# Performance work log

Hardware: AMD Instinct MI355X
Metric: run time of the kernel (lower is better)

Reference implementation:

```python
import jax, jax.numpy as jnp
import numpy as np

ALPHA = 0.2  # LeakyReLU negative slope
NEG_INF = -9e15


def setup_inputs() -> dict:
    key = jax.random.key(0)
    k1, k2, k3, k4 = jax.random.split(key, 4)
    N, IN_F, OUT_F = 8192, 512, 256
    h = jax.random.normal(k1, (N, IN_F), dtype=jnp.float32)
    adj = jax.random.randint(k2, (N, N), 0, 2).astype(jnp.float32)
    # xavier_uniform for torch Linear weights
    limW = float(np.sqrt(6.0 / (IN_F + OUT_F)))
    W = jax.random.uniform(k3, (OUT_F, IN_F), dtype=jnp.float32, minval=-limW, maxval=limW)
    lima = float(np.sqrt(6.0 / (2 * OUT_F + 1)))
    a_vec = jax.random.uniform(k4, (2 * OUT_F,), dtype=jnp.float32, minval=-lima, maxval=lima)
    return {"h": h, "adj": adj, "W": W, "a_vec": a_vec}


def reference(h, adj, W, a_vec):
    # Wh = W(h), torch Linear: h @ W.T  -> [N, out]
    Wh = h @ W.T
    F_out = W.shape[0]
    # e_ij = leakyrelu(a . [Wh_i, Wh_j]) = leakyrelu(a1.Wh_i + a2.Wh_j)
    s_src = Wh @ a_vec[:F_out]   # [N] contribution of row i
    s_dst = Wh @ a_vec[F_out:]   # [N] contribution of col j
    e = jax.nn.leaky_relu(s_src[:, None] + s_dst[None, :], negative_slope=ALPHA)  # [N, N]
    scores = jnp.where(adj > 0, e, jnp.float32(NEG_INF))
    attention = jax.nn.softmax(scores, axis=1)
    # dropout is identity in eval mode
    h_prime = attention @ Wh  # [N, out]
    return h_prime, attention
```

## Files before the change

### kernel.cpp

```cpp
#include <hip/hip_runtime.h>
#include <stdint.h>

#define N_NODES 8192
#define IN_F    512
#define OUT_F   256
#define ALPHA   0.2f

typedef __attribute__((ext_vector_type(8))) short bf16x8;
typedef __attribute__((ext_vector_type(4))) float f32x4;

__device__ __forceinline__ uint32_t f32_to_bf16(float f) {
    union { float f; uint32_t u; } v; v.f = f;
    uint32_t u = v.u;
    return (u + 0x7fffu + ((u >> 16) & 1u)) >> 16;
}

__device__ __forceinline__ void async_copy16(const void* g, void* l) {
    __builtin_amdgcn_global_load_lds(
        (const __attribute__((address_space(1))) uint32_t*)g,
        (__attribute__((address_space(3))) uint32_t*)l, 16, 0, 0);
}

__global__ __launch_bounds__(256) void k0_wvec(
    const float* __restrict__ W, const float* __restrict__ a_vec,
    float* __restrict__ w12)
{
    const int t  = threadIdx.x;
    const int nb = blockIdx.x * 8;
    float a1lo = 0.f, a1hi = 0.f, a2lo = 0.f, a2hi = 0.f;
    #pragma unroll
    for (int q = 0; q < 8; q++) {
        int n = nb + q;
        float lo = W[(size_t)n * IN_F + t];
        float hi = W[(size_t)n * IN_F + t + 256];
        float a1 = a_vec[n], a2 = a_vec[OUT_F + n];
        a1lo = fmaf(lo, a1, a1lo); a1hi = fmaf(hi, a1, a1hi);
        a2lo = fmaf(lo, a2, a2lo); a2hi = fmaf(hi, a2, a2hi);
    }
    atomicAdd(&w12[t], a1lo);       atomicAdd(&w12[t + 256], a1hi);
    atomicAdd(&w12[512 + t], a2lo); atomicAdd(&w12[512 + t + 256], a2hi);
}

__global__ __launch_bounds__(256) void ks_svec(
    const float* __restrict__ h, const float* __restrict__ w12,
    float* __restrict__ s_src, float* __restrict__ s_dst)
{
    __shared__ float sw[1024];
    const int t = threadIdx.x;
    #pragma unroll
    for (int q = 0; q < 4; q++) sw[q * 256 + t] = w12[q * 256 + t];
    __syncthreads();
    const int w = t >> 6, ln = t & 63;
    const int i = blockIdx.x * 4 + w;
    const float* hr = h + (size_t)i * IN_F + ln * 8;
    float4 h0 = *(const float4*)hr;
    float4 h1 = *(const float4*)(hr + 4);
    const float* w1 = sw + ln * 8;
    const float* w2 = sw + 512 + ln * 8;
    float v1 = h0.x*w1[0] + h0.y*w1[1] + h0.z*w1[2] + h0.w*w1[3]
             + h1.x*w1[4] + h1.y*w1[5] + h1.z*w1[6] + h1.w*w1[7];
    float v2 = h0.x*w2[0] + h0.y*w2[1] + h0.z*w2[2] + h0.w*w2[3]
             + h1.x*w2[4] + h1.y*w2[5] + h1.z*w2[6] + h1.w*w2[7];
    #pragma unroll
    for (int off = 32; off >= 1; off >>= 1) {
        v1 += __shfl_xor(v1, off, 64);
        v2 += __shfl_xor(v2, off, 64);
    }
    if (ln == 0) { s_src[i] = v1; s_dst[i] = v2; }
}

__global__ __launch_bounds__(256) void k1_wh_pack(
    const float* __restrict__ h, const float* __restrict__ W,
    uint16_t* __restrict__ whf)
{
    const int n0 = blockIdx.x * 64, i0 = blockIdx.y * 64;
    const int t  = threadIdx.x;
    const int tn = t & 15, tm = t >> 4;

    __shared__ float As[32][65];
    __shared__ float Bs[32][65];

    float acc[4][4];
    #pragma unroll
    for (int i = 0; i < 4; i++)
        #pragma unroll
        for (int j = 0; j < 4; j++) acc[i][j] = 0.f;

    for (int k0 = 0; k0 < IN_F; k0 += 32) {
        __syncthreads();
        #pragma unroll
        for (int q = 0; q < 2; q++) {
            int u   = q * 256 + t;
            int row = u >> 3;
            int kf  = (u & 7) * 4;
            float4 va = *(const float4*)&h[(size_t)(i0 + row) * IN_F + k0 + kf];
            As[kf + 0][row] = va.x; As[kf + 1][row] = va.y;
            As[kf + 2][row] = va.z; As[kf + 3][row] = va.w;
            float4 vb = *(const float4*)&W[(size_t)(n0 + row) * IN_F + k0 + kf];
            Bs[kf + 0][row] = vb.x; Bs[kf + 1][row] = vb.y;
            Bs[kf + 2][row] = vb.z; Bs[kf + 3][row] = vb.w;
        }
        __syncthreads();
        #pragma unroll
        for (int kk = 0; kk < 32; kk++) {
            float a[4], b[4];
            *(float4*)a = *(const float4*)&As[kk][tm * 4];
            *(float4*)b = *(const float4*)&Bs[kk][tn * 4];
            #pragma unroll
            for (int i = 0; i < 4; i++)
                #pragma unroll
                for (int j = 0; j < 4; j++) acc[i][j] = fmaf(a[i], b[j], acc[i][j]);
        }
    }

    #pragma unroll
    for (int ii = 0; ii < 4; ii++) {
        int gr = i0 + tm * 4 + ii;
        int ck = gr >> 5;
        int lr = (gr >> 3) & 3;
        int jj = gr & 7;
        #pragma unroll
        for (int jn = 0; jn < 4; jn++) {
            int gc   = n0 + tn * 4 + jn;
            int c    = ck * 16 + (gc >> 4);
            int lane = (gc & 15) + lr * 16;
            whf[(size_t)c * 512 + lane * 8 + jj] = (uint16_t)f32_to_bf16(acc[ii][jn]);
        }
    }
}

__global__ __launch_bounds__(256) void k2_mask_l(
    const float* __restrict__ adj, const float* __restrict__ s_src,
    const float* __restrict__ s_dst, uint64_t* __restrict__ mask,
    float* __restrict__ l_out)
{
    const int i = blockIdx.x;
    const int t = threadIdx.x, w = t >> 6, ln = t & 63;
    const float si = s_src[i];
    const float4* rowv = (const float4*)(adj + (size_t)i * N_NODES);
    const float4* sdv  = (const float4*)s_dst;
    float acc = 0.f;
    #pragma unroll 2
    for (int it = 0; it < 8; it++) {
        int jb = it * 4 + w;
        int v4 = jb * 64 + ln;
        float4 a  = rowv[v4];
        float4 sd = sdv[v4];
        uint64_t b0 = __ballot(a.x > 0.f);
        uint64_t b1 = __ballot(a.y > 0.f);
        uint64_t b2 = __ballot(a.z > 0.f);
        uint64_t b3 = __ballot(a.w > 0.f);
        if (ln == 0) {
            uint64_t* mw = mask + (size_t)i * 128 + jb * 4;
            mw[0] = b0; mw[1] = b1; mw[2] = b2; mw[3] = b3;
        }
        float x, e;
        x = si + sd.x; e = fmaxf(x, ALPHA * x); if (a.x > 0.f) acc += __expf(e);
        x = si + sd.y; e = fmaxf(x, ALPHA * x); if (a.y > 0.f) acc += __expf(e);
        x = si + sd.z; e = fmaxf(x, ALPHA * x); if (a.z > 0.f) acc += __expf(e);
        x = si + sd.w; e = fmaxf(x, ALPHA * x); if (a.w > 0.f) acc += __expf(e);
    }
    #pragma unroll
    for (int off = 32; off >= 1; off >>= 1) acc += __shfl_xor(acc, off, 64);
    __shared__ float red[4];
    if (ln == 0) red[w] = acc;
    __syncthreads();
    if (t == 0) l_out[i] = (red[0] + red[1]) + (red[2] + red[3]);
}

__global__ __launch_bounds__(256) void k3_att_gemm(
    const uint64_t* __restrict__ mask, const float* __restrict__ s_src,
    const float* __restrict__ s_dst, const float* __restrict__ l_in,
    const uint16_t* __restrict__ whf, float* __restrict__ att_out,
    float* __restrict__ partial)
{
    const int rb = blockIdx.x, jc = blockIdx.y;
    const int i0 = rb * 32, jbase = jc * 2048;
    const int t = threadIdx.x, w = t >> 6, ln = t & 63;
    const int mh = w & 1, nh = w >> 1;

    __shared__ uint16_t whf_lds[16384];
    __shared__ uint64_t mw[2][32][4];
    __shared__ float    sd[2][64];
    __shared__ float    ssrc[32], invl[32];

    if (t < 32) { ssrc[t] = s_src[i0 + t]; invl[t] = 1.0f / l_in[i0 + t]; }
    if (t < 64) sd[0][t] = s_dst[jbase + t];
    if (t >= 64 && t < 192) {
        int r = (t - 64) >> 2, ph = t & 3;
        mw[0][r][ph] = mask[(size_t)(i0 + r) * 128 + (jbase >> 8) * 4 + ph];
    }

    f32x4 acc[8];
    #pragma unroll
    for (int b = 0; b < 8; b++) acc[b] = (f32x4){0.f, 0.f, 0.f, 0.f};

    const int m   = mh * 16 + (ln & 15);
    const int kof = (ln >> 4) * 8;

    int cur = 0;
    for (int it = 0; it < 32; it++) {
        const int j0 = jbase + it * 64;
        __syncthreads();

        const uint16_t* src = whf + (size_t)(j0 >> 5) * 8192;
        #pragma unroll
        for (int q = 0; q < 8; q++) {
            int c = w * 8 + q;
            async_copy16(src + (size_t)c * 512 + ln * 8, whf_lds + c * 512);
        }

        uint64_t mwv[4];
        #pragma unroll
        for (int ph = 0; ph < 4; ph++) mwv[ph] = mw[cur][m][ph];
        float sim = ssrc[m], il = invl[m];
        int bbase = ((it & 3) << 4) + (kof >> 2);
        float p[2][8];
        #pragma unroll
        for (int ks = 0; ks < 2; ks++) {
            #pragma unroll
            for (int jj = 0; jj < 8; jj++) {
                float x  = sim + sd[cur][ks * 32 + kof + jj];
                float e  = fmaxf(x, ALPHA * x);
                float pe = __expf(e) * il;
                int bidx = bbase + ks * 8 + (jj >> 2);
                p[ks][jj] = ((mwv[jj & 3] >> bidx) & 1ull) ? pe : 0.f;
            }
        }

        if (nh == 0) {
            float* go = att_out + (size_t)(i0 + m) * N_NODES + j0 + kof;
            __builtin_nontemporal_store(*(f32x4*)&p[0][0], (f32x4*)go);
            __builtin_nontemporal_store(*(f32x4*)&p[0][4], (f32x4*)(go + 4));
            __builtin_nontemporal_store(*(f32x4*)&p[1][0], (f32x4*)(go + 32));
            __builtin_nontemporal_store(*(f32x4*)&p[1][4], (f32x4*)(go + 36));
        }

        bf16x8 af[2];
        #pragma unroll
        for (int ks = 0; ks < 2; ks++) {
            union { bf16x8 v; uint32_t u[4]; } pk;
            #pragma unroll
            for (int q = 0; q < 4; q++)
                pk.u[q] = f32_to_bf16(p[ks][2 * q]) | (f32_to_bf16(p[ks][2 * q + 1]) << 16);
            af[ks] = pk.v;
        }

        if (it < 31) {
            int jn = j0 + 64;
            if (t < 64) sd[cur ^ 1][t] = s_dst[jn + t];
            else if (t < 192) {
                int r = (t - 64) >> 2, ph = t & 3;
                mw[cur ^ 1][r][ph] = mask[(size_t)(i0 + r) * 128 + (jn >> 8) * 4 + ph];
            }
        }
        __syncthreads();

        #pragma unroll
        for (int ks = 0; ks < 2; ks++) {
            #pragma unroll
            for (int nl = 0; nl < 8; nl++) {
                int nt = nh * 8 + nl;
                bf16x8 bfr = *(const bf16x8*)(whf_lds + (size_t)(ks * 16 + nt) * 512 + ln * 8);
                acc[nl] = __builtin_amdgcn_mfma_f32_16x16x32_bf16(af[ks], bfr, acc[nl], 0, 0, 0);
            }
        }
        cur ^= 1;
    }

    float* pbase = partial + (size_t)jc * ((size_t)N_NODES * OUT_F);
    int gr0 = i0 + mh * 16 + (ln >> 4) * 4;
    #pragma unroll
    for (int nl = 0; nl < 8; nl++) {
        int gc = nh * 128 + nl * 16 + (ln & 15);
        #pragma unroll
        for (int r = 0; r < 4; r++)
            pbase[(size_t)(gr0 + r) * OUT_F + gc] = acc[nl][r];
    }
}

__global__ __launch_bounds__(256) void k4_reduce(
    const float* __restrict__ partial, float* __restrict__ hp)
{
    const size_t S = (size_t)N_NODES * OUT_F;
    int idx = (blockIdx.x * 256 + threadIdx.x) * 4;
    float4 a = *(const float4*)(partial + idx);
    float4 b = *(const float4*)(partial + S + idx);
    float4 c = *(const float4*)(partial + 2 * S + idx);
    float4 d = *(const float4*)(partial + 3 * S + idx);
    float4 o;
    o.x = (a.x + b.x) + (c.x + d.x);
    o.y = (a.y + b.y) + (c.y + d.y);
    o.z = (a.z + b.z) + (c.z + d.z);
    o.w = (a.w + b.w) + (c.w + d.w);
    *(float4*)(hp + idx) = o;
}

extern "C" void kernel_launch(void* const* d_in, const int* in_sizes, int n_in,
                              void* d_out, int out_size, void* d_ws, size_t ws_size,
                              hipStream_t stream) {
    (void)in_sizes; (void)n_in; (void)out_size; (void)ws_size;
    const float* h     = (const float*)d_in[0];
    const float* adj   = (const float*)d_in[1];
    const float* W     = (const float*)d_in[2];
    const float* a_vec = (const float*)d_in[3];

    char* ws = (char*)d_ws;
    uint16_t* whf  = (uint16_t*)(ws);
    uint64_t* mask = (uint64_t*)(ws + ((size_t)4 << 20));
    float* partial = (float*)(ws + ((size_t)12 << 20));
    float* w12     = (float*)(ws + ((size_t)44 << 20));
    float* s_src   = (float*)(ws + ((size_t)44 << 20) + 16384);
    float* s_dst   = (float*)(ws + ((size_t)44 << 20) + 16384 + 32768);
    float* l_buf   = (float*)(ws + ((size_t)44 << 20) + 16384 + 65536);

    float* hp  = (float*)d_out;
    float* att = hp + (size_t)N_NODES * OUT_F;

    hipMemsetAsync(w12, 0, 4096, stream);
    k0_wvec<<<32, 256, 0, stream>>>(W, a_vec, w12);
    ks_svec<<<2048, 256, 0, stream>>>(h, w12, s_src, s_dst);
    k1_wh_pack<<<dim3(4, 128), 256, 0, stream>>>(h, W, whf);
    k2_mask_l<<<8192, 256, 0, stream>>>(adj, s_src, s_dst, mask, l_buf);
    k3_att_gemm<<<dim3(256, 4), 256, 0, stream>>>(mask, s_src, s_dst, l_buf, whf, att, partial);
    k4_reduce<<<2048, 256, 0, stream>>>(partial, hp);
}
```

Measured before the change: 645.0 us.

## Split K across waves in attention GEMM and drop LDS staging of Wh

The attention-GEMM kernel now splits each 64-column chunk across wave pairs along K instead of along N. Each wave computes its own 32 attention values and runs all 16 output column tiles, reading Wh fragments straight from global memory rather than through an async LDS copy. This removes the per-iteration block barriers and the redundant computation of softmax values, and adds a final LDS reduction between the two K halves. The trade-off is more global/L2 traffic for Wh, more accumulator registers (16 tiles, with an occupancy hint of 4), and padding of the k1 shared tiles to 68.

```diff
diff --git a/kernel.cpp b/kernel.cpp
--- a/kernel.cpp
+++ b/kernel.cpp
@@ -13,12 +13,6 @@
     union { float f; uint32_t u; } v; v.f = f;
     uint32_t u = v.u;
     return (u + 0x7fffu + ((u >> 16) & 1u)) >> 16;
-}
-
-__device__ __forceinline__ void async_copy16(const void* g, void* l) {
-    __builtin_amdgcn_global_load_lds(
-        (const __attribute__((address_space(1))) uint32_t*)g,
-        (__attribute__((address_space(3))) uint32_t*)l, 16, 0, 0);
 }
 
 __global__ __launch_bounds__(256) void k0_wvec(
@@ -77,8 +71,8 @@
     const int t  = threadIdx.x;
     const int tn = t & 15, tm = t >> 4;
 
-    __shared__ float As[32][65];
-    __shared__ float Bs[32][65];
+    __shared__ float As[32][68];
+    __shared__ float Bs[32][68];
 
     float acc[4][4];
     #pragma unroll
@@ -168,7 +162,7 @@
     if (t == 0) l_out[i] = (red[0] + red[1]) + (red[2] + red[3]);
 }
 
-__global__ __launch_bounds__(256) void k3_att_gemm(
+__global__ __launch_bounds__(256, 4) void k3_att_gemm(
     const uint64_t* __restrict__ mask, const float* __restrict__ s_src,
     const float* __restrict__ s_dst, const float* __restrict__ l_in,
     const uint16_t* __restrict__ whf, float* __restrict__ att_out,
@@ -177,105 +171,84 @@
     const int rb = blockIdx.x, jc = blockIdx.y;
     const int i0 = rb * 32, jbase = jc * 2048;
     const int t = threadIdx.x, w = t >> 6, ln = t & 63;
-    const int mh = w & 1, nh = w >> 1;
-
-    __shared__ uint16_t whf_lds[16384];
-    __shared__ uint64_t mw[2][32][4];
-    __shared__ float    sd[2][64];
-    __shared__ float    ssrc[32], invl[32];
-
-    if (t < 32) { ssrc[t] = s_src[i0 + t]; invl[t] = 1.0f / l_in[i0 + t]; }
-    if (t < 64) sd[0][t] = s_dst[jbase + t];
-    if (t >= 64 && t < 192) {
-        int r = (t - 64) >> 2, ph = t & 3;
-        mw[0][r][ph] = mask[(size_t)(i0 + r) * 128 + (jbase >> 8) * 4 + ph];
-    }
-
-    f32x4 acc[8];
-    #pragma unroll
-    for (int b = 0; b < 8; b++) acc[b] = (f32x4){0.f, 0.f, 0.f, 0.f};
+    const int mh = w & 1, kh = w >> 1;
 
     const int m   = mh * 16 + (ln & 15);
     const int kof = (ln >> 4) * 8;
-
-    int cur = 0;
+    const int gi  = i0 + m;
+
+    const float sim = s_src[gi];
+    const float il  = 1.0f / l_in[gi];
+
+    f32x4 acc[16];
+    #pragma unroll
+    for (int b = 0; b < 16; b++) acc[b] = (f32x4){0.f, 0.f, 0.f, 0.f};
+
+    const uint64_t* mrow = mask + (size_t)gi * 128 + (jbase >> 8) * 4;
+    uint64_t mwv[4];
+
     for (int it = 0; it < 32; it++) {
         const int j0 = jbase + it * 64;
-        __syncthreads();
-
-        const uint16_t* src = whf + (size_t)(j0 >> 5) * 8192;
-        #pragma unroll
-        for (int q = 0; q < 8; q++) {
-            int c = w * 8 + q;
-            async_copy16(src + (size_t)c * 512 + ln * 8, whf_lds + c * 512);
-        }
-
-        uint64_t mwv[4];
-        #pragma unroll
-        for (int ph = 0; ph < 4; ph++) mwv[ph] = mw[cur][m][ph];
-        float sim = ssrc[m], il = invl[m];
-        int bbase = ((it & 3) << 4) + (kof >> 2);
-        float p[2][8];
-        #pragma unroll
-        for (int ks = 0; ks < 2; ks++) {
+
+        if ((it & 3) == 0) {
+            const uint64_t* mp = mrow + (it >> 2) * 4;
+            mwv[0] = mp[0]; mwv[1] = mp[1]; mwv[2] = mp[2]; mwv[3] = mp[3];
+        }
+
+        const float* sp = s_dst + j0 + kh * 32 + kof;
+        float4 sd0 = *(const float4*)sp;
+        float4 sd1 = *(const float4*)(sp + 4);
+        float sdv[8] = {sd0.x, sd0.y, sd0.z, sd0.w, sd1.x, sd1.y, sd1.z, sd1.w};
+
+        const int bbase = ((it & 3) << 4) + (kh << 3) + (kof >> 2);
+        float p[8];
+        #pragma unroll
+        for (int jj = 0; jj < 8; jj++) {
+            float x  = sim + sdv[jj];
+            float e  = fmaxf(x, ALPHA * x);
+            float pe = __expf(e) * il;
+            int bidx = bbase + (jj >> 2);
+            p[jj] = ((mwv[jj & 3] >> bidx) & 1ull) ? pe : 0.f;
+        }
+
+        float* go = att_out + (size_t)gi * N_NODES + j0 + kh * 32 + kof;
+        __builtin_nontemporal_store(*(f32x4*)&p[0], (f32x4*)go);
+        __builtin_nontemporal_store(*(f32x4*)&p[4], (f32x4*)(go + 4));
+
+        union { bf16x8 v; uint32_t u[4]; } pk;
+        #pragma unroll
+        for (int q = 0; q < 4; q++)
+            pk.u[q] = f32_to_bf16(p[2 * q]) | (f32_to_bf16(p[2 * q + 1]) << 16);
+        bf16x8 af = pk.v;
+
+        const uint16_t* src = whf + (((size_t)(j0 >> 5) + kh) << 13) + ln * 8;
+        #pragma unroll
+        for (int nl = 0; nl < 16; nl++) {
+            bf16x8 bfr = *(const bf16x8*)(src + nl * 512);
+            acc[nl] = __builtin_amdgcn_mfma_f32_16x16x32_bf16(af, bfr, acc[nl], 0, 0, 0);
+        }
+    }
+
+    __shared__ float red[2][16][257];
+    const int lr = (ln >> 4) * 4;
+    if (kh == 1) {
+        #pragma unroll
+        for (int nl = 0; nl < 16; nl++)
             #pragma unroll
-            for (int jj = 0; jj < 8; jj++) {
-                float x  = sim + sd[cur][ks * 32 + kof + jj];
-                float e  = fmaxf(x, ALPHA * x);
-                float pe = __expf(e) * il;
-                int bidx = bbase + ks * 8 + (jj >> 2);
-                p[ks][jj] = ((mwv[jj & 3] >> bidx) & 1ull) ? pe : 0.f;
-            }
-        }
-
-        if (nh == 0) {
-            float* go = att_out + (size_t)(i0 + m) * N_NODES + j0 + kof;
-            __builtin_nontemporal_store(*(f32x4*)&p[0][0], (f32x4*)go);
-            __builtin_nontemporal_store(*(f32x4*)&p[0][4], (f32x4*)(go + 4));
-            __builtin_nontemporal_store(*(f32x4*)&p[1][0], (f32x4*)(go + 32));
-            __builtin_nontemporal_store(*(f32x4*)&p[1][4], (f32x4*)(go + 36));
-        }
-
-        bf16x8 af[2];
-        #pragma unroll
-        for (int ks = 0; ks < 2; ks++) {
-            union { bf16x8 v; uint32_t u[4]; } pk;
+            for (int r = 0; r < 4; r++)
+                red[mh][lr + r][nl * 16 + (ln & 15)] = acc[nl][r];
+    }
+    __syncthreads();
+    if (kh == 0) {
+        float* pbase = partial + (size_t)jc * ((size_t)N_NODES * OUT_F);
+        const int gr0 = i0 + mh * 16 + lr;
+        #pragma unroll
+        for (int nl = 0; nl < 16; nl++) {
+            int gc = nl * 16 + (ln & 15);
             #pragma unroll
-            for (int q = 0; q < 4; q++)
-                pk.u[q] = f32_to_bf16(p[ks][2 * q]) | (f32_to_bf16(p[ks][2 * q + 1]) << 16);
-            af[ks] = pk.v;
-        }
-
-        if (it < 31) {
-            int jn = j0 + 64;
-            if (t < 64) sd[cur ^ 1][t] = s_dst[jn + t];
-            else if (t < 192) {
-                int r = (t - 64) >> 2, ph = t & 3;
-                mw[cur ^ 1][r][ph] = mask[(size_t)(i0 + r) * 128 + (jn >> 8) * 4 + ph];
-            }
-        }
-        __syncthreads();
-
-        #pragma unroll
-        for (int ks = 0; ks < 2; ks++) {
-            #pragma unroll
-            for (int nl = 0; nl < 8; nl++) {
-                int nt = nh * 8 + nl;
-                bf16x8 bfr = *(const bf16x8*)(whf_lds + (size_t)(ks * 16 + nt) * 512 + ln * 8);
-                acc[nl] = __builtin_amdgcn_mfma_f32_16x16x32_bf16(af[ks], bfr, acc[nl], 0, 0, 0);
-            }
-        }
-        cur ^= 1;
-    }
-
-    float* pbase = partial + (size_t)jc * ((size_t)N_NODES * OUT_F);
-    int gr0 = i0 + mh * 16 + (ln >> 4) * 4;
-    #pragma unroll
-    for (int nl = 0; nl < 8; nl++) {
-        int gc = nh * 128 + nl * 16 + (ln & 15);
-        #pragma unroll
-        for (int r = 0; r < 4; r++)
-            pbase[(size_t)(gr0 + r) * OUT_F + gc] = acc[nl][r];
+            for (int r = 0; r < 4; r++)
+                pbase[(size_t)(gr0 + r) * OUT_F + gc] = acc[nl][r] + red[mh][lr + r][gc];
+        }
     }
 }
 
```

New measurement: 727.4 us. 12.8% more time.
